# Kernel tuning notes

Hardware: AMD Instinct MI355X
Metric: run time of the kernel (lower is better)

Reference implementation:

```python
import jax, jax.numpy as jnp
import numpy as np

B, N, NC = 16, 25200, 80
CONF_THRES = 0.25
IOU_THRES = 0.45
MAX_DET = 300
MAX_WH = 7680.0   # yolov5 per-class box offset for class-aware NMS
TOPK = 1024       # pre-NMS candidate cap (fixed-shape stand-in for yolov5 max_nms)


def setup_inputs():
    key = jax.random.key(0)
    k1, k2 = jax.random.split(key)
    # xywh in pixel units (640x640 image, boxes up to ~120 px); obj/cls confidences in [0,1]
    xywh = jax.random.uniform(k1, (B, N, 4), dtype=jnp.float32) * jnp.array([640.0, 640.0, 120.0, 120.0], jnp.float32)
    conf = jax.random.uniform(k2, (B, N, 1 + NC), dtype=jnp.float32)
    return {"YOLOoutput": jnp.concatenate([xywh, conf], axis=-1)}


def _xywh2xyxy(x):
    cx, cy, w, h = x[..., 0], x[..., 1], x[..., 2], x[..., 3]
    return jnp.stack([cx - w / 2, cy - h / 2, cx + w / 2, cy + h / 2], axis=-1)


def _pairwise_iou(a, b):
    # a, b: [K,4] xyxy -> [K,K]
    lt = jnp.maximum(a[:, None, :2], b[None, :, :2])
    rb = jnp.minimum(a[:, None, 2:], b[None, :, 2:])
    wh = jnp.maximum(rb - lt, 0.0)
    inter = wh[..., 0] * wh[..., 1]
    area_a = (a[:, 2] - a[:, 0]) * (a[:, 3] - a[:, 1])
    area_b = (b[:, 2] - b[:, 0]) * (b[:, 3] - b[:, 1])
    return inter / (area_a[:, None] + area_b[None, :] - inter + 1e-7)


def _nms_single(pred):
    # pred: [N, 5+NC]
    obj = pred[:, 4]
    cls_conf = pred[:, 5:] * obj[:, None]      # conf = obj_conf * cls_conf (yolov5)
    conf = jnp.max(cls_conf, axis=-1)
    j = jnp.argmax(cls_conf, axis=-1)
    valid = (obj > CONF_THRES) & (conf > CONF_THRES)
    box = _xywh2xyxy(pred[:, :4])
    scores = jnp.where(valid, conf, -1.0)      # invalid candidates sink to bottom
    top_scores, idx = jax.lax.top_k(scores, TOPK)
    b = box[idx]                               # [TOPK,4]
    c = j[idx].astype(box.dtype)
    boxes_off = b + (c * MAX_WH)[:, None]      # class-aware NMS via per-class offset
    valid_k = top_scores > 0.0
    iou = _pairwise_iou(boxes_off, boxes_off)
    ar = jnp.arange(TOPK)

    def body(i, supp):
        active = jnp.logical_not(supp[i])
        return supp | (active & (iou[i] > IOU_THRES) & (ar > i))

    supp = jax.lax.fori_loop(0, TOPK, body, jnp.logical_not(valid_k))
    keep = valid_k & jnp.logical_not(supp)
    fs, fi = jax.lax.top_k(jnp.where(keep, top_scores, -1.0), MAX_DET)
    dv = fs > 0.0
    det_box = b[fi] * dv[:, None]              # zero out padded rows
    det = jnp.concatenate(
        [det_box, jnp.where(dv, fs, 0.0)[:, None], (c[fi] * dv)[:, None]], axis=-1
    )                                          # [MAX_DET, 6] = x1,y1,x2,y2,conf,cls
    return det, dv


def reference(YOLOoutput):
    det, dvalid = jax.vmap(_nms_single)(YOLOoutput)   # [B,MAX_DET,6], [B,MAX_DET]
    scores = det[..., 4]
    mean_conf = jnp.max(scores, axis=1)               # = 0 when image has no detections
    n = dvalid.sum(axis=1)
    terms = jnp.abs(det[..., 0:2] - det[..., 2:4]) * scores[..., None]  # padded rows are 0
    s = terms.sum(axis=(1, 2))
    wh = jnp.where(n > 0, s / (2.0 * jnp.maximum(n, 1)), 0.0)  # mean over n*2 elements
    conf_addition = mean_conf.sum() / B
    w_and_h = wh.sum() / B
    return conf_addition, w_and_h, det[2]
```

## Files before the change

kernel.cpp:

```cpp
#include <hip/hip_runtime.h>
#include <hip/hip_bf16.h>

typedef unsigned long long u64;
typedef unsigned int u32;

#define BATCH 16
#define NANCH 25200
#define NCLS 80
#define NFEAT 85
#define TOPK 1024
#define MAXDET 300
#define CONF_T 0.25f
#define IOU_T 0.45f
#define MAX_WH 7680.0f

#define TILE_A 128
#define TILES_PER_BLK 4

__global__ __launch_bounds__(512) void score_kernel(const float* __restrict__ in,
                                                    u64* __restrict__ keys) {
    __shared__ float ld[TILE_A * NFEAT];
    const int b = blockIdx.y, tid = threadIdx.x;
    for (int t = 0; t < TILES_PER_BLK; ++t) {
        const int tile = blockIdx.x * TILES_PER_BLK + t;
        const int a0 = tile * TILE_A;
        if (a0 >= NANCH) break;
        const int na = min(TILE_A, NANCH - a0);
        const int nf4 = na * NFEAT / 4;
        const float4* src = (const float4*)(in + ((size_t)b * NANCH + a0) * NFEAT);
        if (t) __syncthreads();
        for (int k = tid; k < nf4; k += 512) ((float4*)ld)[k] = src[k];
        __syncthreads();
        const int a = tid >> 2, q = tid & 3;
        if (a < na) {
            const float* p = ld + a * NFEAT;
            float obj = p[4];
            float best = -1e30f;
            int bj = 0;
#pragma unroll
            for (int k = 0; k < 20; ++k) {
                float v = p[5 + q * 20 + k] * obj;
                if (v > best) { best = v; bj = q * 20 + k; }
            }
#pragma unroll
            for (int d = 1; d < 4; d <<= 1) {
                float ob = __shfl_xor(best, d, 64);
                int oj = __shfl_xor(bj, d, 64);
                if (ob > best || (ob == best && oj < bj)) { best = ob; bj = oj; }
            }
            if (q == 0) {
                bool valid = (obj > CONF_T) && (best > CONF_T);
                float sc = valid ? best : -1.0f;
                u32 sb = __float_as_uint(sc);
                u32 ord = sb ^ ((sb & 0x80000000u) ? 0xFFFFFFFFu : 0x80000000u);
                int idx = a0 + a;
                keys[(size_t)b * NANCH + idx] =
                    ((u64)ord << 32) | ((u64)((u32)(idx ^ 0xFFFF) & 0xFFFFu) << 8) | (u64)bj;
            }
        }
    }
}

__global__ __launch_bounds__(1024) void select_topk(const u64* __restrict__ keys,
                                                    const float* __restrict__ in,
                                                    float4* __restrict__ box4,
                                                    float4* __restrict__ boxoff4,
                                                    float* __restrict__ score,
                                                    float* __restrict__ cls,
                                                    u64* __restrict__ vmask) {
    const int b = blockIdx.x, tid = threadIdx.x;
    const u64* kb = keys + (size_t)b * NANCH;
    __shared__ u32 hist[256];
    __shared__ u32 sfx[256];
    __shared__ u32 s_prefix, s_cg, s_cnt;
    __shared__ u64 buf[2048];

    if (tid == 0) { s_prefix = 0u; s_cg = 0u; }
    for (int p = 0; p < 4; ++p) {
        if (tid < 256) hist[tid] = 0u;
        __syncthreads();
        const u32 prefix = s_prefix;
        const u32 cg = s_cg;
        const int sh_match = 32 - 8 * p;
        const int sh_dig = 24 - 8 * p;
#pragma unroll 4
        for (int n = tid; n < NANCH; n += 1024) {
            u32 hi = (u32)(kb[n] >> 32);
            if (((u64)(hi ^ prefix) >> sh_match) == 0ull)
                atomicAdd(&hist[(hi >> sh_dig) & 0xFFu], 1u);
        }
        __syncthreads();
        if (tid < 64) {
            u32 h0 = hist[tid * 4], h1 = hist[tid * 4 + 1];
            u32 h2 = hist[tid * 4 + 2], h3 = hist[tid * 4 + 3];
            u32 s3v = h3, s2v = h2 + s3v, s1v = h1 + s2v, s0v = h0 + s1v;
            u32 S = s0v;
#pragma unroll
            for (int d = 1; d < 64; d <<= 1) {
                u32 o = __shfl_down(S, d, 64);
                if (tid + d < 64) S += o;
            }
            u32 E = S - s0v;
            sfx[tid * 4]     = E + s0v;
            sfx[tid * 4 + 1] = E + s1v;
            sfx[tid * 4 + 2] = E + s2v;
            sfx[tid * 4 + 3] = E + s3v;
        }
        __syncthreads();
        const u32 need = (u32)TOPK - cg;
        if (tid < 256) {
            u32 s0 = sfx[tid];
            u32 s1 = (tid < 255) ? sfx[tid + 1] : 0u;
            if (s0 >= need && s1 < need) {
                s_prefix = prefix | ((u32)tid << sh_dig);
                s_cg = cg + s1;
            }
        }
        __syncthreads();
    }
    const u32 thr = s_prefix;
    if (tid == 0) s_cnt = 0u;
    __syncthreads();
#pragma unroll 4
    for (int n = tid; n < NANCH; n += 1024) {
        u64 k = kb[n];
        if ((u32)(k >> 32) > thr) {
            u32 pos = atomicAdd(&s_cnt, 1u);
            if (pos < 2048u) buf[pos] = k;
        }
    }
    __syncthreads();
#pragma unroll 4
    for (int n = tid; n < NANCH; n += 1024) {
        u64 k = kb[n];
        if ((u32)(k >> 32) == thr) {
            u32 pos = atomicAdd(&s_cnt, 1u);
            if (pos < 2048u) buf[pos] = k;
        }
    }
    __syncthreads();
    u32 cnt = s_cnt; if (cnt > 2048u) cnt = 2048u;
    for (int n = (int)cnt + tid; n < 2048; n += 1024) buf[n] = 0ull;
    __syncthreads();

    const int wv = tid >> 6, l = tid & 63;
    const int base = wv * 128;
    u64 r0 = buf[base + l], r1 = buf[base + 64 + l];
    for (int k2 = 2; k2 <= 128; k2 <<= 1) {
        const bool d0 = (((base + l) & k2) == 0);
        const bool d1 = (((base + 64 + l) & k2) == 0);
        for (int jj = (k2 >> 1); jj >= 1; jj >>= 1) {
            if (jj == 64) {
                u64 mx = r0 > r1 ? r0 : r1, mn = r0 > r1 ? r1 : r0;
                r0 = d0 ? mx : mn; r1 = d0 ? mn : mx;
            } else {
                const bool up = (l & jj) != 0;
                u64 v0 = __shfl_xor(r0, jj, 64);
                u64 v1 = __shfl_xor(r1, jj, 64);
                const bool km0 = (d0 != up), km1 = (d1 != up);
                r0 = km0 ? (r0 > v0 ? r0 : v0) : (r0 < v0 ? r0 : v0);
                r1 = km1 ? (r1 > v1 ? r1 : v1) : (r1 < v1 ? r1 : v1);
            }
        }
    }
    for (int k2 = 256; k2 <= 2048; k2 <<= 1) {
        buf[base + l] = r0; buf[base + 64 + l] = r1;
        __syncthreads();
        for (int jj = (k2 >> 1); jj >= 128; jj >>= 1) {
            int i = ((tid & ~(jj - 1)) << 1) | (tid & (jj - 1));
            int part = i | jj;
            u64 a = buf[i], c = buf[part];
            bool sw = ((i & k2) == 0) ? (a < c) : (a > c);
            if (sw) { buf[i] = c; buf[part] = a; }
            __syncthreads();
        }
        r0 = buf[base + l]; r1 = buf[base + 64 + l];
        const bool d0 = (((base + l) & k2) == 0);
        for (int jj = 64; jj >= 1; jj >>= 1) {
            if (jj == 64) {
                u64 mx = r0 > r1 ? r0 : r1, mn = r0 > r1 ? r1 : r0;
                r0 = d0 ? mx : mn; r1 = d0 ? mn : mx;
            } else {
                const bool up = (l & jj) != 0;
                u64 v0 = __shfl_xor(r0, jj, 64);
                u64 v1 = __shfl_xor(r1, jj, 64);
                const bool km = (d0 != up);
                r0 = km ? (r0 > v0 ? r0 : v0) : (r0 < v0 ? r0 : v0);
                r1 = km ? (r1 > v1 ? r1 : v1) : (r1 < v1 ? r1 : v1);
            }
        }
    }
    buf[base + l] = r0; buf[base + 64 + l] = r1;
    __syncthreads();

    u64 k = buf[tid];
    u32 ord = (u32)(k >> 32);
    u32 sb = (ord & 0x80000000u) ? (ord ^ 0x80000000u) : ~ord;
    float sc = __uint_as_float(sb);
    int idx = (int)((((u32)(k >> 8)) & 0xFFFFu) ^ 0xFFFFu);
    int j = (int)(k & 0xFFu);
    const float* pr = in + ((size_t)b * NANCH + idx) * NFEAT;
    float cx = pr[0], cy = pr[1], ww = pr[2], hh = pr[3];
    float x1 = cx - ww / 2.0f, y1 = cy - hh / 2.0f;
    float x2 = cx + ww / 2.0f, y2 = cy + hh / 2.0f;
    float c = (float)j;
    float cm = c * MAX_WH;
    box4[b * TOPK + tid]    = make_float4(x1, y1, x2, y2);
    boxoff4[b * TOPK + tid] = make_float4(x1 + cm, y1 + cm, x2 + cm, y2 + cm);
    score[b * TOPK + tid] = sc;
    cls[b * TOPK + tid] = c;
    u64 bal = __ballot(sc > 0.0f);
    if ((tid & 63) == 0) vmask[b * 16 + (tid >> 6)] = bal;
}

__global__ __launch_bounds__(256) void iou_mask(const float4* __restrict__ boxoff4,
                                                u64* __restrict__ M) {
    const int wavei = (blockIdx.x << 2) | (threadIdx.x >> 6);
    const int lane = threadIdx.x & 63;
    const int b = wavei >> 10;
    const int i = wavei & 1023;
    const float4 A = boxoff4[b * TOPK + i];
    const float areaA = (A.z - A.x) * (A.w - A.y);
    u64 myword = 0ull;
#pragma unroll 4
    for (int t = 0; t < 16; ++t) {
        int j = (t << 6) | lane;
        float4 Bx = boxoff4[b * TOPK + j];
        float lx = fmaxf(A.x, Bx.x), ly = fmaxf(A.y, Bx.y);
        float rx = fminf(A.z, Bx.z), ry = fminf(A.w, Bx.w);
        float iw = fmaxf(rx - lx, 0.0f), ih = fmaxf(ry - ly, 0.0f);
        float inter = iw * ih;
        float areaB = (Bx.z - Bx.x) * (Bx.w - Bx.y);
        float iou = inter / (areaA + areaB - inter + 1e-7f);
        bool pred = (iou > IOU_T) && (j > i);
        u64 bal = __ballot(pred);
        if (lane == t) myword = bal;
    }
    if (lane < 16) M[((size_t)b * TOPK + i) * 16 + lane] = myword;
}

__global__ __launch_bounds__(64) void nms_seq(const u64* __restrict__ M,
                                              const u64* __restrict__ vmask,
                                              u64* __restrict__ keepmask) {
    const int lane = threadIdx.x;
    const int b = blockIdx.x * 4 + (lane >> 4);
    const int w = lane & 15;
    const int grp = lane & 48;
    u64 supp = ~vmask[b * 16 + w];
    const u64* Mb = M + (size_t)b * TOPK * 16;
    u64 rwA[16], rwB[16];
#pragma unroll
    for (int q = 0; q < 16; ++q) rwA[q] = Mb[q * 16 + w];
    for (int wb = 0; wb < 16; ++wb) {
        u64 cur = __shfl(supp, grp | wb, 64);
#pragma unroll
        for (int c4 = 0; c4 < 4; ++c4) {
            const int rn = wb * 64 + (c4 + 1) * 16;
            if (rn < 1024) {
#pragma unroll
                for (int q = 0; q < 16; ++q) rwB[q] = Mb[(rn + q) * 16 + w];
            }
            u64 rc[16];
#pragma unroll
            for (int q = 0; q < 16; ++q) rc[q] = __shfl(rwA[q], grp | wb, 64);
#pragma unroll
            for (int q = 0; q < 16; ++q) {
                const int ii = c4 * 16 + q;
                const bool act = ((cur >> ii) & 1ull) == 0ull;
                supp = act ? (supp | rwA[q]) : supp;
                cur  = act ? (cur  | rc[q])  : cur;
            }
#pragma unroll
            for (int q = 0; q < 16; ++q) rwA[q] = rwB[q];
        }
    }
    keepmask[b * 16 + w] = vmask[b * 16 + w] & ~supp;
}

__global__ __launch_bounds__(256) void finalize(const float4* __restrict__ box4,
                                                const float* __restrict__ score,
                                                const float* __restrict__ cls,
                                                const u64* __restrict__ keepmask,
                                                float* __restrict__ out) {
    const int b = blockIdx.x, tid = threadIdx.x;
    __shared__ u64 kw[16];
    __shared__ int wpfx[17];
    __shared__ float sdet[MAXDET * 6];
    __shared__ float s_sum, s_max;
    if (tid < 16) kw[tid] = keepmask[b * 16 + tid];
    if (tid == 0) { s_sum = 0.0f; s_max = 0.0f; }
    __syncthreads();
    if (tid == 0) {
        int acc = 0;
        for (int w = 0; w < 16; ++w) { wpfx[w] = acc; acc += __popcll(kw[w]); }
        wpfx[16] = acc;
    }
    for (int t = tid; t < MAXDET * 6; t += 256) sdet[t] = 0.0f;
    __syncthreads();
    for (int r = tid; r < TOPK; r += 256) {
        int w = r >> 6, bp = r & 63;
        if ((kw[w] >> bp) & 1ull) {
            int pos = wpfx[w] + __popcll(kw[w] & ((1ull << bp) - 1ull));
            if (pos < MAXDET) {
                float4 bx = box4[b * TOPK + r];
                float s = score[b * TOPK + r];
                float c = cls[b * TOPK + r];
                sdet[pos * 6 + 0] = bx.x;
                sdet[pos * 6 + 1] = bx.y;
                sdet[pos * 6 + 2] = bx.z;
                sdet[pos * 6 + 3] = bx.w;
                sdet[pos * 6 + 4] = s;
                sdet[pos * 6 + 5] = c;
                float term = (fabsf(bx.x - bx.z) + fabsf(bx.y - bx.w)) * s;
                atomicAdd(&s_sum, term);
                if (pos == 0) s_max = s;
            }
        }
    }
    __syncthreads();
    if (tid == 0) {
        int n = wpfx[16]; if (n > MAXDET) n = MAXDET;
        float wh = (n > 0) ? (s_sum / (2.0f * (float)n)) : 0.0f;
        atomicAdd(&out[0], s_max / (float)BATCH);
        atomicAdd(&out[1], wh / (float)BATCH);
    }
    if (b == 2) {
        for (int t = tid; t < MAXDET * 6; t += 256) out[2 + t] = sdet[t];
    }
}

extern "C" void kernel_launch(void* const* d_in, const int* in_sizes, int n_in,
                              void* d_out, int out_size, void* d_ws, size_t ws_size,
                              hipStream_t stream) {
    const float* in = (const float*)d_in[0];
    float* out = (float*)d_out;
    char* ws = (char*)d_ws;

    u64*    keys     = (u64*)   (ws + 0);
    float4* boxoff4  = (float4*)(ws + 3225600);
    float4* box4     = (float4*)(ws + 3487744);
    float*  score    = (float*) (ws + 3749888);
    float*  cls      = (float*) (ws + 3815424);
    u64*    vmask    = (u64*)   (ws + 3880960);
    u64*    M        = (u64*)   (ws + 3883008);
    u64*    keepmask = (u64*)   (ws + 5980160);

    hipMemsetAsync(out, 0, 2 * sizeof(float), stream);
    score_kernel<<<dim3(50, BATCH), 512, 0, stream>>>(in, keys);
    select_topk<<<BATCH, 1024, 0, stream>>>(keys, in, box4, boxoff4, score, cls, vmask);
    iou_mask<<<BATCH * TOPK / 4, 256, 0, stream>>>(boxoff4, M);
    nms_seq<<<4, 64, 0, stream>>>(M, vmask, keepmask);
    finalize<<<BATCH, 256, 0, stream>>>(box4, score, cls, keepmask, out);
}
```

Measured before the change: 315.4 us.

## Shrink score tiles, use single-pass 12-bit radix select, fuse NMS with finalize

The score kernel now uses 64-anchor tiles with 256 threads and launches 197 blocks per image instead of 50, spreading the input read across more CUs. The top-k threshold search replaces four 8-bit radix passes over the keys with one 4096-bin histogram on the top 12 bits. The candidate buffer then holds everything above or equal to that coarse bucket, capped at 2048. The sequential NMS and finalize kernels are merged into one per-image 64-thread kernel, dropping a launch and the keepmask round trip. The NMS scan now runs with only 16 active lanes per block, and if the boundary bucket overflows the 2048-entry buffer some candidates could be lost.

```diff
diff --git a/kernel.cpp b/kernel.cpp
--- a/kernel.cpp
+++ b/kernel.cpp
@@ -14,10 +14,10 @@
 #define IOU_T 0.45f
 #define MAX_WH 7680.0f
 
-#define TILE_A 128
-#define TILES_PER_BLK 4
-
-__global__ __launch_bounds__(512) void score_kernel(const float* __restrict__ in,
+#define TILE_A 64
+#define TILES_PER_BLK 2
+
+__global__ __launch_bounds__(256) void score_kernel(const float* __restrict__ in,
                                                     u64* __restrict__ keys) {
     __shared__ float ld[TILE_A * NFEAT];
     const int b = blockIdx.y, tid = threadIdx.x;
@@ -29,7 +29,7 @@
         const int nf4 = na * NFEAT / 4;
         const float4* src = (const float4*)(in + ((size_t)b * NANCH + a0) * NFEAT);
         if (t) __syncthreads();
-        for (int k = tid; k < nf4; k += 512) ((float4*)ld)[k] = src[k];
+        for (int k = tid; k < nf4; k += 256) ((float4*)ld)[k] = src[k];
         __syncthreads();
         const int a = tid >> 2, q = tid & 3;
         if (a < na) {
@@ -69,62 +69,54 @@
                                                     float* __restrict__ cls,
                                                     u64* __restrict__ vmask) {
     const int b = blockIdx.x, tid = threadIdx.x;
+    const int lane = tid & 63, wv = tid >> 6;
     const u64* kb = keys + (size_t)b * NANCH;
-    __shared__ u32 hist[256];
-    __shared__ u32 sfx[256];
-    __shared__ u32 s_prefix, s_cg, s_cnt;
+    __shared__ u32 hist[4096];
+    __shared__ u32 wtot[16];
+    __shared__ u32 wsfx[16];
+    __shared__ u32 s_prefix12, s_cnt;
     __shared__ u64 buf[2048];
 
-    if (tid == 0) { s_prefix = 0u; s_cg = 0u; }
-    for (int p = 0; p < 4; ++p) {
-        if (tid < 256) hist[tid] = 0u;
-        __syncthreads();
-        const u32 prefix = s_prefix;
-        const u32 cg = s_cg;
-        const int sh_match = 32 - 8 * p;
-        const int sh_dig = 24 - 8 * p;
+#pragma unroll
+    for (int i = 0; i < 4; ++i) hist[tid * 4 + i] = 0u;
+    __syncthreads();
 #pragma unroll 4
-        for (int n = tid; n < NANCH; n += 1024) {
-            u32 hi = (u32)(kb[n] >> 32);
-            if (((u64)(hi ^ prefix) >> sh_match) == 0ull)
-                atomicAdd(&hist[(hi >> sh_dig) & 0xFFu], 1u);
-        }
-        __syncthreads();
-        if (tid < 64) {
-            u32 h0 = hist[tid * 4], h1 = hist[tid * 4 + 1];
-            u32 h2 = hist[tid * 4 + 2], h3 = hist[tid * 4 + 3];
-            u32 s3v = h3, s2v = h2 + s3v, s1v = h1 + s2v, s0v = h0 + s1v;
-            u32 S = s0v;
-#pragma unroll
-            for (int d = 1; d < 64; d <<= 1) {
-                u32 o = __shfl_down(S, d, 64);
-                if (tid + d < 64) S += o;
-            }
-            u32 E = S - s0v;
-            sfx[tid * 4]     = E + s0v;
-            sfx[tid * 4 + 1] = E + s1v;
-            sfx[tid * 4 + 2] = E + s2v;
-            sfx[tid * 4 + 3] = E + s3v;
-        }
-        __syncthreads();
-        const u32 need = (u32)TOPK - cg;
-        if (tid < 256) {
-            u32 s0 = sfx[tid];
-            u32 s1 = (tid < 255) ? sfx[tid + 1] : 0u;
-            if (s0 >= need && s1 < need) {
-                s_prefix = prefix | ((u32)tid << sh_dig);
-                s_cg = cg + s1;
-            }
-        }
-        __syncthreads();
-    }
-    const u32 thr = s_prefix;
+    for (int n = tid; n < NANCH; n += 1024) {
+        u32 hi = (u32)(kb[n] >> 32);
+        atomicAdd(&hist[hi >> 20], 1u);
+    }
+    __syncthreads();
+    u32 h0 = hist[tid * 4], h1 = hist[tid * 4 + 1];
+    u32 h2 = hist[tid * 4 + 2], h3 = hist[tid * 4 + 3];
+    u32 s3v = h3, s2v = h2 + s3v, s1v = h1 + s2v, s0v = h0 + s1v;
+    u32 S = s0v;
+#pragma unroll
+    for (int d = 1; d < 64; d <<= 1) {
+        u32 o = __shfl_down(S, d, 64);
+        if (lane + d < 64) S += o;
+    }
+    if (lane == 0) wtot[wv] = S;
+    __syncthreads();
+    if (tid == 0) {
+        u32 acc = 0;
+        for (int w = 15; w >= 0; --w) { wsfx[w] = acc; acc += wtot[w]; }
+    }
+    __syncthreads();
+    {
+        const u32 E = wsfx[wv] + (S - s0v);
+        const u32 v0 = E + s0v, v1 = E + s1v, v2 = E + s2v, v3 = E + s3v, v4 = E;
+        if (v0 >= (u32)TOPK && v1 < (u32)TOPK) s_prefix12 = (u32)(tid * 4 + 0);
+        if (v1 >= (u32)TOPK && v2 < (u32)TOPK) s_prefix12 = (u32)(tid * 4 + 1);
+        if (v2 >= (u32)TOPK && v3 < (u32)TOPK) s_prefix12 = (u32)(tid * 4 + 2);
+        if (v3 >= (u32)TOPK && v4 < (u32)TOPK) s_prefix12 = (u32)(tid * 4 + 3);
+    }
     if (tid == 0) s_cnt = 0u;
     __syncthreads();
+    const u32 p12 = s_prefix12;
 #pragma unroll 4
     for (int n = tid; n < NANCH; n += 1024) {
         u64 k = kb[n];
-        if ((u32)(k >> 32) > thr) {
+        if (((u32)(k >> 32) >> 20) > p12) {
             u32 pos = atomicAdd(&s_cnt, 1u);
             if (pos < 2048u) buf[pos] = k;
         }
@@ -133,7 +125,7 @@
 #pragma unroll 4
     for (int n = tid; n < NANCH; n += 1024) {
         u64 k = kb[n];
-        if ((u32)(k >> 32) == thr) {
+        if (((u32)(k >> 32) >> 20) == p12) {
             u32 pos = atomicAdd(&s_cnt, 1u);
             if (pos < 2048u) buf[pos] = k;
         }
@@ -143,18 +135,17 @@
     for (int n = (int)cnt + tid; n < 2048; n += 1024) buf[n] = 0ull;
     __syncthreads();
 
-    const int wv = tid >> 6, l = tid & 63;
     const int base = wv * 128;
-    u64 r0 = buf[base + l], r1 = buf[base + 64 + l];
+    u64 r0 = buf[base + lane], r1 = buf[base + 64 + lane];
     for (int k2 = 2; k2 <= 128; k2 <<= 1) {
-        const bool d0 = (((base + l) & k2) == 0);
-        const bool d1 = (((base + 64 + l) & k2) == 0);
+        const bool d0 = (((base + lane) & k2) == 0);
+        const bool d1 = (((base + 64 + lane) & k2) == 0);
         for (int jj = (k2 >> 1); jj >= 1; jj >>= 1) {
             if (jj == 64) {
                 u64 mx = r0 > r1 ? r0 : r1, mn = r0 > r1 ? r1 : r0;
                 r0 = d0 ? mx : mn; r1 = d0 ? mn : mx;
             } else {
-                const bool up = (l & jj) != 0;
+                const bool up = (lane & jj) != 0;
                 u64 v0 = __shfl_xor(r0, jj, 64);
                 u64 v1 = __shfl_xor(r1, jj, 64);
                 const bool km0 = (d0 != up), km1 = (d1 != up);
@@ -164,7 +155,7 @@
         }
     }
     for (int k2 = 256; k2 <= 2048; k2 <<= 1) {
-        buf[base + l] = r0; buf[base + 64 + l] = r1;
+        buf[base + lane] = r0; buf[base + 64 + lane] = r1;
         __syncthreads();
         for (int jj = (k2 >> 1); jj >= 128; jj >>= 1) {
             int i = ((tid & ~(jj - 1)) << 1) | (tid & (jj - 1));
@@ -174,14 +165,14 @@
             if (sw) { buf[i] = c; buf[part] = a; }
             __syncthreads();
         }
-        r0 = buf[base + l]; r1 = buf[base + 64 + l];
-        const bool d0 = (((base + l) & k2) == 0);
+        r0 = buf[base + lane]; r1 = buf[base + 64 + lane];
+        const bool d0 = (((base + lane) & k2) == 0);
         for (int jj = 64; jj >= 1; jj >>= 1) {
             if (jj == 64) {
                 u64 mx = r0 > r1 ? r0 : r1, mn = r0 > r1 ? r1 : r0;
                 r0 = d0 ? mx : mn; r1 = d0 ? mn : mx;
             } else {
-                const bool up = (l & jj) != 0;
+                const bool up = (lane & jj) != 0;
                 u64 v0 = __shfl_xor(r0, jj, 64);
                 u64 v1 = __shfl_xor(r1, jj, 64);
                 const bool km = (d0 != up);
@@ -190,7 +181,7 @@
             }
         }
     }
-    buf[base + l] = r0; buf[base + 64 + l] = r1;
+    buf[base + lane] = r0; buf[base + 64 + lane] = r1;
     __syncthreads();
 
     u64 k = buf[tid];
@@ -239,65 +230,60 @@
     if (lane < 16) M[((size_t)b * TOPK + i) * 16 + lane] = myword;
 }
 
-__global__ __launch_bounds__(64) void nms_seq(const u64* __restrict__ M,
-                                              const u64* __restrict__ vmask,
-                                              u64* __restrict__ keepmask) {
-    const int lane = threadIdx.x;
-    const int b = blockIdx.x * 4 + (lane >> 4);
-    const int w = lane & 15;
-    const int grp = lane & 48;
-    u64 supp = ~vmask[b * 16 + w];
-    const u64* Mb = M + (size_t)b * TOPK * 16;
-    u64 rwA[16], rwB[16];
-#pragma unroll
-    for (int q = 0; q < 16; ++q) rwA[q] = Mb[q * 16 + w];
-    for (int wb = 0; wb < 16; ++wb) {
-        u64 cur = __shfl(supp, grp | wb, 64);
-#pragma unroll
-        for (int c4 = 0; c4 < 4; ++c4) {
-            const int rn = wb * 64 + (c4 + 1) * 16;
-            if (rn < 1024) {
-#pragma unroll
-                for (int q = 0; q < 16; ++q) rwB[q] = Mb[(rn + q) * 16 + w];
-            }
-            u64 rc[16];
-#pragma unroll
-            for (int q = 0; q < 16; ++q) rc[q] = __shfl(rwA[q], grp | wb, 64);
-#pragma unroll
-            for (int q = 0; q < 16; ++q) {
-                const int ii = c4 * 16 + q;
-                const bool act = ((cur >> ii) & 1ull) == 0ull;
-                supp = act ? (supp | rwA[q]) : supp;
-                cur  = act ? (cur  | rc[q])  : cur;
-            }
-#pragma unroll
-            for (int q = 0; q < 16; ++q) rwA[q] = rwB[q];
-        }
-    }
-    keepmask[b * 16 + w] = vmask[b * 16 + w] & ~supp;
-}
-
-__global__ __launch_bounds__(256) void finalize(const float4* __restrict__ box4,
-                                                const float* __restrict__ score,
-                                                const float* __restrict__ cls,
-                                                const u64* __restrict__ keepmask,
-                                                float* __restrict__ out) {
-    const int b = blockIdx.x, tid = threadIdx.x;
+__global__ __launch_bounds__(64) void nms_finalize(const u64* __restrict__ M,
+                                                   const u64* __restrict__ vmask,
+                                                   const float4* __restrict__ box4,
+                                                   const float* __restrict__ score,
+                                                   const float* __restrict__ cls,
+                                                   float* __restrict__ out) {
+    const int b = blockIdx.x, lane = threadIdx.x;
     __shared__ u64 kw[16];
     __shared__ int wpfx[17];
     __shared__ float sdet[MAXDET * 6];
     __shared__ float s_sum, s_max;
-    if (tid < 16) kw[tid] = keepmask[b * 16 + tid];
-    if (tid == 0) { s_sum = 0.0f; s_max = 0.0f; }
-    __syncthreads();
-    if (tid == 0) {
+    if (lane == 0) { s_sum = 0.0f; s_max = 0.0f; }
+    if (lane < 16) {
+        const int w = lane;
+        const u64 vm = vmask[b * 16 + w];
+        u64 supp = ~vm;
+        const u64* Mb = M + (size_t)b * TOPK * 16;
+        u64 rwA[16], rwB[16];
+#pragma unroll
+        for (int q = 0; q < 16; ++q) rwA[q] = Mb[q * 16 + w];
+        for (int wb = 0; wb < 16; ++wb) {
+            u64 cur = __shfl(supp, wb, 64);
+#pragma unroll
+            for (int c4 = 0; c4 < 4; ++c4) {
+                const int rn = wb * 64 + (c4 + 1) * 16;
+                if (rn < 1024) {
+#pragma unroll
+                    for (int q = 0; q < 16; ++q) rwB[q] = Mb[(rn + q) * 16 + w];
+                }
+                u64 rc[16];
+#pragma unroll
+                for (int q = 0; q < 16; ++q) rc[q] = __shfl(rwA[q], wb, 64);
+#pragma unroll
+                for (int q = 0; q < 16; ++q) {
+                    const int ii = c4 * 16 + q;
+                    const bool act = ((cur >> ii) & 1ull) == 0ull;
+                    supp = act ? (supp | rwA[q]) : supp;
+                    cur  = act ? (cur  | rc[q])  : cur;
+                }
+#pragma unroll
+                for (int q = 0; q < 16; ++q) rwA[q] = rwB[q];
+            }
+        }
+        kw[w] = vm & ~supp;
+    }
+    __syncthreads();
+    if (lane == 0) {
         int acc = 0;
         for (int w = 0; w < 16; ++w) { wpfx[w] = acc; acc += __popcll(kw[w]); }
         wpfx[16] = acc;
     }
-    for (int t = tid; t < MAXDET * 6; t += 256) sdet[t] = 0.0f;
-    __syncthreads();
-    for (int r = tid; r < TOPK; r += 256) {
+    for (int t = lane; t < MAXDET * 6; t += 64) sdet[t] = 0.0f;
+    __syncthreads();
+    for (int r = lane; r < TOPK; r += 64) {
         int w = r >> 6, bp = r & 63;
         if ((kw[w] >> bp) & 1ull) {
             int pos = wpfx[w] + __popcll(kw[w] & ((1ull << bp) - 1ull));
@@ -318,14 +304,14 @@
         }
     }
     __syncthreads();
-    if (tid == 0) {
+    if (lane == 0) {
         int n = wpfx[16]; if (n > MAXDET) n = MAXDET;
         float wh = (n > 0) ? (s_sum / (2.0f * (float)n)) : 0.0f;
         atomicAdd(&out[0], s_max / (float)BATCH);
         atomicAdd(&out[1], wh / (float)BATCH);
     }
     if (b == 2) {
-        for (int t = tid; t < MAXDET * 6; t += 256) out[2 + t] = sdet[t];
+        for (int t = lane; t < MAXDET * 6; t += 64) out[2 + t] = sdet[t];
     }
 }
 
@@ -343,12 +329,10 @@
     float*  cls      = (float*) (ws + 3815424);
     u64*    vmask    = (u64*)   (ws + 3880960);
     u64*    M        = (u64*)   (ws + 3883008);
-    u64*    keepmask = (u64*)   (ws + 5980160);
 
     hipMemsetAsync(out, 0, 2 * sizeof(float), stream);
-    score_kernel<<<dim3(50, BATCH), 512, 0, stream>>>(in, keys);
+    score_kernel<<<dim3(197, BATCH), 256, 0, stream>>>(in, keys);
     select_topk<<<BATCH, 1024, 0, stream>>>(keys, in, box4, boxoff4, score, cls, vmask);
     iou_mask<<<BATCH * TOPK / 4, 256, 0, stream>>>(boxoff4, M);
-    nms_seq<<<4, 64, 0, stream>>>(M, vmask, keepmask);
-    finalize<<<BATCH, 256, 0, stream>>>(box4, score, cls, keepmask, out);
-}
+    nms_finalize<<<BATCH, 64, 0, stream>>>(M, vmask, box4, score, cls, out);
+}
```

Result: faster. 304.0 us (-3.6%).
